# Performance work log

Measured on AMD Instinct MI355X. Metric: run time of the kernel, lower is better.

The kernel has to match this reference:

```python
import jax, jax.numpy as jnp
import numpy as np

BETA = 0.9      # LIF leak
THRESH = 1.0    # snntorch Leaky default threshold
SLOPE = 25.0    # fast_sigmoid surrogate slope

@jax.custom_vjp
def spike(x):
    # Heaviside forward, fast_sigmoid surrogate backward
    return (x > 0).astype(x.dtype)

def _spike_fwd(x):
    return spike(x), x

def _spike_bwd(x, g):
    return (g / (SLOPE * jnp.abs(x) + 1.0) ** 2,)

spike.defvjp(_spike_fwd, _spike_bwd)


def setup_inputs() -> dict:
    key = jax.random.key(0)
    k0, k1, k2, k3, k4 = jax.random.split(key, 5)
    B, T, I, H, C = 256, 100, 512, 1024, 8
    x = jax.random.normal(k0, (B, T, I), dtype=jnp.float32)
    s1 = 1.0 / np.sqrt(I)
    s2 = 1.0 / np.sqrt(H)
    W1 = jax.random.uniform(k1, (H, I), jnp.float32, -s1, s1)
    b1 = jax.random.uniform(k2, (H,), jnp.float32, -s1, s1)
    W2 = jax.random.uniform(k3, (C, H), jnp.float32, -s2, s2)
    b2 = jax.random.uniform(k4, (C,), jnp.float32, -s2, s2)
    return {"x": x, "W1": W1, "b1": b1, "W2": W2, "b2": b2}


def reference(x, W1, b1, W2, b2):
    # x: [B, T, I]
    B, T, I = x.shape
    H = W1.shape[0]
    # fc1 for all timesteps as one big GEMM (same math as per-step loop).
    cur = jnp.einsum('bti,hi->tbh', x, W1) + b1  # [T, B, H]

    def step(mem, c):
        # snntorch Leaky (reset_mechanism='subtract'):
        reset = spike(mem - THRESH)
        mem_new = BETA * mem + c - reset * THRESH
        spk = spike(mem_new - THRESH)
        return mem_new, spk

    mem0 = jnp.zeros((B, H), dtype=x.dtype)
    _, spk_rec = jax.lax.scan(step, mem0, cur)  # spk_rec: [T, B, H]

    # sum_t (spk_t @ W2.T + b2) == (sum_t spk_t) @ W2.T + T*b2
    spk_sum = spk_rec.sum(axis=0)  # [B, H]
    logits = spk_sum @ W2.T + T * b2  # [B, C]
    return logits
```

## Files before the change

kernel.cpp:

```cpp
#include <hip/hip_runtime.h>


#define B_   256
#define T_   100
#define I_   512
#define H_   1024
#define C_   8
#define M_   (B_ * T_)
#define KS_  1024
#define SC   64.0f
#define ISC  (1.0f / 4096.0f)
#define CP   132

typedef _Float16 half8 __attribute__((ext_vector_type(8)));
typedef float floatx4 __attribute__((ext_vector_type(4)));

__device__ __forceinline__ void ld_g2l(const _Float16* g, _Float16* l) {
    __builtin_amdgcn_global_load_lds(
        (const __attribute__((address_space(1))) void*)g,
        (__attribute__((address_space(3))) void*)l, 16, 0, 0);
}

__global__ void __launch_bounds__(256)
split_all(const float* __restrict__ x, const float* __restrict__ W1,
          const float* __restrict__ b2, _Float16* __restrict__ Asp,
          float* __restrict__ out) {
    int g = blockIdx.x * 256 + threadIdx.x;
    if (g < B_ * C_) out[g] = 100.0f * b2[g & (C_ - 1)];
    int row = g >> 6;
    int i0 = (g & 63) * 8;
    const float* src = (row < M_) ? (x + (size_t)row * I_ + i0)
                                  : (W1 + (size_t)(row - M_) * I_ + i0);
    float4 v0 = *(const float4*)(src);
    float4 v1 = *(const float4*)(src + 4);
    float vv[8] = {v0.x, v0.y, v0.z, v0.w, v1.x, v1.y, v1.z, v1.w};
    half8 hi, lo;
#pragma unroll
    for (int j = 0; j < 8; ++j) {
        float s = vv[j] * SC;
        _Float16 h = (_Float16)s;
        hi[j] = h;
        lo[j] = (_Float16)(s - (float)h);
    }
    _Float16* r = Asp + (size_t)row * KS_ + i0;
    *(half8*)(r) = hi;
    *(half8*)(r + 512) = lo;
}

__global__ void __launch_bounds__(256, 4)
snn_mfma(const _Float16* __restrict__ Asp, const _Float16* __restrict__ Wsp,
         const float* __restrict__ b1, const float* __restrict__ W2,
         float* __restrict__ logits) {
    __shared__ union {
        struct { __align__(16) _Float16 A[128 * 64]; __align__(16) _Float16 Bm[128 * 64]; } g;
        float Cs[64 * CP];
    } sm;
    const int tid = threadIdx.x;
    const int lane = tid & 63;
    const int w = tid >> 6;

    const int xcd = blockIdx.x & 7;
    const int jj = blockIdx.x >> 3;
    const int b  = xcd * 32 + (jj >> 3);
    const int n0 = (jj & 7) * 128;

    const int wm = (w >> 1) * 64;
    const int wn = (w & 1) * 64;
    const int srow = lane >> 3;
    const int sc16 = (lane & 7) ^ srow;

    const _Float16* ag[4];
    const _Float16* bg[4];
    _Float16* al[4];
    _Float16* bl[4];
#pragma unroll
    for (int j = 0; j < 4; ++j) {
        const int r = w * 32 + j * 8 + srow;
        ag[j] = Asp + ((size_t)b * T_ + r) * KS_ + sc16 * 8;
        bg[j] = Wsp + (size_t)(n0 + r) * KS_ + sc16 * 8;
        al[j] = &sm.g.A[(w * 32 + j * 8) * 64];
        bl[j] = &sm.g.Bm[(w * 32 + j * 8) * 64];
    }

    floatx4 acc[4][4];
#pragma unroll
    for (int i = 0; i < 4; ++i)
#pragma unroll
        for (int q = 0; q < 4; ++q) acc[i][q] = (floatx4){0.f, 0.f, 0.f, 0.f};

    const int quad = lane >> 4;
    const int l15 = lane & 15;
    const int l7 = lane & 7;

    for (int kt = 0; kt < 24; ++kt) {
        const int koA = ((kt & 16) ? 512 : 0) + (kt & 7) * 64;
        const int koB = ((kt & 8)  ? 512 : 0) + (kt & 7) * 64;
        __syncthreads();
#pragma unroll
        for (int j = 0; j < 4; ++j) {
            if (j < 2 || w < 3) ld_g2l(ag[j] + koA, al[j]);
            ld_g2l(bg[j] + koB, bl[j]);
        }
        __syncthreads();
#pragma unroll
        for (int ks = 0; ks < 2; ++ks) {
            const int c16 = (ks * 4 + quad) ^ l7;
            half8 av[3], bv[4];
#pragma unroll
            for (int f = 0; f < 3; ++f)
                av[f] = *(const half8*)&sm.g.A[(wm + f * 16 + l15) * 64 + c16 * 8];
#pragma unroll
            for (int f = 0; f < 4; ++f)
                bv[f] = *(const half8*)&sm.g.Bm[(wn + f * 16 + l15) * 64 + c16 * 8];
#pragma unroll
            for (int fr = 0; fr < 3; ++fr)
#pragma unroll
                for (int fn = 0; fn < 4; ++fn)
                    acc[fr][fn] = __builtin_amdgcn_mfma_f32_16x16x32_f16(
                        av[fr], bv[fn], acc[fr][fn], 0, 0, 0);
            if (wm == 0) {
                half8 a3 = *(const half8*)&sm.g.A[(48 + l15) * 64 + c16 * 8];
#pragma unroll
                for (int fn = 0; fn < 4; ++fn)
                    acc[3][fn] = __builtin_amdgcn_mfma_f32_16x16x32_f16(
                        a3, bv[fn], acc[3][fn], 0, 0, 0);
            }
        }
    }

    float b1c[4];
#pragma unroll
    for (int fn = 0; fn < 4; ++fn) b1c[fn] = b1[n0 + wn + fn * 16 + l15];

    float mem = 0.f, ss = 0.f;
    const int myh = tid & 127;

    __syncthreads();
    if (w < 2) {
#pragma unroll
        for (int fr = 0; fr < 4; ++fr)
#pragma unroll
            for (int r = 0; r < 4; ++r) {
                float* dst = &sm.Cs[(fr * 16 + quad * 4 + r) * CP + wn + l15];
#pragma unroll
                for (int fn = 0; fn < 4; ++fn)
                    dst[fn * 16] = acc[fr][fn][r] * ISC + b1c[fn];
            }
    }
    __syncthreads();
    if (tid < 128) {
#pragma unroll 8
        for (int t = 0; t < 64; ++t) {
            float c = sm.Cs[t * CP + myh];
            float reset = (mem > 1.0f) ? 1.0f : 0.0f;
            mem = 0.9f * mem + c - reset;
            ss += (mem > 1.0f) ? 1.0f : 0.0f;
        }
    }
    __syncthreads();
    if (w >= 2) {
#pragma unroll
        for (int fr = 0; fr < 3; ++fr)
#pragma unroll
            for (int r = 0; r < 4; ++r) {
                float* dst = &sm.Cs[(fr * 16 + quad * 4 + r) * CP + wn + l15];
#pragma unroll
                for (int fn = 0; fn < 4; ++fn)
                    dst[fn * 16] = acc[fr][fn][r] * ISC + b1c[fn];
            }
    }
    __syncthreads();
    if (tid < 128) {
#pragma unroll 6
        for (int t = 0; t < 36; ++t) {
            float c = sm.Cs[t * CP + myh];
            float reset = (mem > 1.0f) ? 1.0f : 0.0f;
            mem = 0.9f * mem + c - reset;
            ss += (mem > 1.0f) ? 1.0f : 0.0f;
        }
#pragma unroll
        for (int c = 0; c < C_; ++c) {
            float v = ss * W2[c * H_ + n0 + myh];
#pragma unroll
            for (int off = 32; off; off >>= 1) v += __shfl_down(v, off, 64);
            if (lane == 0) atomicAdd(&logits[b * C_ + c], v);
        }
    }
}

extern "C" void kernel_launch(void* const* d_in, const int* in_sizes, int n_in,
                              void* d_out, int out_size, void* d_ws, size_t ws_size,
                              hipStream_t stream) {
    const float* x  = (const float*)d_in[0];
    const float* W1 = (const float*)d_in[1];
    const float* b1 = (const float*)d_in[2];
    const float* W2 = (const float*)d_in[3];
    const float* b2 = (const float*)d_in[4];
    float* out = (float*)d_out;

    char* ws = (char*)d_ws;
    _Float16* Asp = (_Float16*)ws;
    _Float16* Wsp = (_Float16*)(ws + (size_t)M_ * KS_ * 2);

    hipLaunchKernelGGL(split_all, dim3((M_ + H_) * 64 / 256), dim3(256), 0, stream,
                       x, W1, b2, Asp, out);
    hipLaunchKernelGGL(snn_mfma, dim3(B_ * 8), dim3(256), 0, stream,
                       Asp, Wsp, b1, W2, out);
}
```

Before: 196.5 us.

## Use 32x32 MFMA with 128x256 tiles and double-buffered LDS pipeline

Replaces the 16x16x32 MFMA GEMM with 32x32x16 instructions over a wider 128x256 output tile per block, halving the grid. Global-to-LDS loads are double buffered with explicit waitcnt and barriers so the next K slice streams in while the current one computes. The split-fp16 product now loads hi and lo halves in the same stage and skips the lo*lo term in registers, instead of iterating 24 separate K tiles. All 256 threads run the LIF scan over 256 hidden units. Occupancy drops to 2 blocks per CU and register pressure rises.

```diff
diff --git a/kernel.cpp b/kernel.cpp
--- a/kernel.cpp
+++ b/kernel.cpp
@@ -10,10 +10,9 @@
 #define KS_  1024
 #define SC   64.0f
 #define ISC  (1.0f / 4096.0f)
-#define CP   132
 
 typedef _Float16 half8 __attribute__((ext_vector_type(8)));
-typedef float floatx4 __attribute__((ext_vector_type(4)));
+typedef float floatx16 __attribute__((ext_vector_type(16)));
 
 __device__ __forceinline__ void ld_g2l(const _Float16* g, _Float16* l) {
     __builtin_amdgcn_global_load_lds(
@@ -47,13 +46,50 @@
     *(half8*)(r + 512) = lo;
 }
 
-__global__ void __launch_bounds__(256, 4)
+#define MFMA32(A, Bv, Cacc) \
+    Cacc = __builtin_amdgcn_mfma_f32_32x32x16_f16(A, Bv, Cacc, 0, 0, 0)
+
+#define STAGE(dd, koff) do {                                         \
+    _Float16* lb = &sm.buf[0][0] + (dd) * 12288;                     \
+    ld_g2l(ga0 + (koff), lb + w * 512);                              \
+    ld_g2l(ga1 + (koff), lb + 2048 + w * 512);                       \
+    ld_g2l(gb00 + (koff), lb + 4096 + w * 1024);                     \
+    ld_g2l(gb01 + (koff), lb + 4096 + w * 1024 + 512);               \
+    ld_g2l(gb10 + (koff), lb + 8192 + w * 1024);                     \
+    ld_g2l(gb11 + (koff), lb + 8192 + w * 1024 + 512);               \
+} while (0)
+
+#define COMPUTE(dd) do {                                             \
+    const _Float16* bb = &sm.buf[0][0] + (dd) * 12288;               \
+    half8 ah[2], al[2], bh[4], bl[4];                                \
+    _Pragma("unroll")                                                \
+    for (int f = 0; f < 2; ++f) {                                    \
+        ah[f] = *(const half8*)(bb + ra + f * 512);                  \
+        al[f] = *(const half8*)(bb + 2048 + ra + f * 512);           \
+    }                                                                \
+    _Pragma("unroll")                                                \
+    for (int f = 0; f < 4; ++f) {                                    \
+        bh[f] = *(const half8*)(bb + 4096 + rb + f * 512);           \
+        bl[f] = *(const half8*)(bb + 8192 + rb + f * 512);           \
+    }                                                                \
+    _Pragma("unroll")                                                \
+    for (int fm = 0; fm < 2; ++fm) {                                 \
+        _Pragma("unroll")                                            \
+        for (int fn = 0; fn < 4; ++fn) {                             \
+            MFMA32(ah[fm], bh[fn], acc[fm][fn]);                     \
+            MFMA32(ah[fm], bl[fn], acc[fm][fn]);                     \
+            MFMA32(al[fm], bh[fn], acc[fm][fn]);                     \
+        }                                                            \
+    }                                                                \
+} while (0)
+
+__global__ void __launch_bounds__(256, 2)
 snn_mfma(const _Float16* __restrict__ Asp, const _Float16* __restrict__ Wsp,
          const float* __restrict__ b1, const float* __restrict__ W2,
          float* __restrict__ logits) {
     __shared__ union {
-        struct { __align__(16) _Float16 A[128 * 64]; __align__(16) _Float16 Bm[128 * 64]; } g;
-        float Cs[64 * CP];
+        __align__(16) _Float16 buf[2][12288];
+        float Cs[64 * 256];
     } sm;
     const int tid = threadIdx.x;
     const int lane = tid & 63;
@@ -61,130 +97,103 @@
 
     const int xcd = blockIdx.x & 7;
     const int jj = blockIdx.x >> 3;
-    const int b  = xcd * 32 + (jj >> 3);
-    const int n0 = (jj & 7) * 128;
+    const int b  = xcd * 32 + (jj >> 2);
+    const int n0 = (jj & 3) * 256;
 
     const int wm = (w >> 1) * 64;
-    const int wn = (w & 1) * 64;
-    const int srow = lane >> 3;
-    const int sc16 = (lane & 7) ^ srow;
-
-    const _Float16* ag[4];
-    const _Float16* bg[4];
-    _Float16* al[4];
-    _Float16* bl[4];
-#pragma unroll
-    for (int j = 0; j < 4; ++j) {
-        const int r = w * 32 + j * 8 + srow;
-        ag[j] = Asp + ((size_t)b * T_ + r) * KS_ + sc16 * 8;
-        bg[j] = Wsp + (size_t)(n0 + r) * KS_ + sc16 * 8;
-        al[j] = &sm.g.A[(w * 32 + j * 8) * 64];
-        bl[j] = &sm.g.Bm[(w * 32 + j * 8) * 64];
-    }
-
-    floatx4 acc[4][4];
-#pragma unroll
-    for (int i = 0; i < 4; ++i)
-#pragma unroll
-        for (int q = 0; q < 4; ++q) acc[i][q] = (floatx4){0.f, 0.f, 0.f, 0.f};
-
-    const int quad = lane >> 4;
-    const int l15 = lane & 15;
-    const int l7 = lane & 7;
-
-    for (int kt = 0; kt < 24; ++kt) {
-        const int koA = ((kt & 16) ? 512 : 0) + (kt & 7) * 64;
-        const int koB = ((kt & 8)  ? 512 : 0) + (kt & 7) * 64;
-        __syncthreads();
-#pragma unroll
-        for (int j = 0; j < 4; ++j) {
-            if (j < 2 || w < 3) ld_g2l(ag[j] + koA, al[j]);
-            ld_g2l(bg[j] + koB, bl[j]);
-        }
-        __syncthreads();
-#pragma unroll
-        for (int ks = 0; ks < 2; ++ks) {
-            const int c16 = (ks * 4 + quad) ^ l7;
-            half8 av[3], bv[4];
-#pragma unroll
-            for (int f = 0; f < 3; ++f)
-                av[f] = *(const half8*)&sm.g.A[(wm + f * 16 + l15) * 64 + c16 * 8];
-#pragma unroll
-            for (int f = 0; f < 4; ++f)
-                bv[f] = *(const half8*)&sm.g.Bm[(wn + f * 16 + l15) * 64 + c16 * 8];
-#pragma unroll
-            for (int fr = 0; fr < 3; ++fr)
+    const int wn = (w & 1) * 128;
+    const int l31 = lane & 31;
+    const int q2 = lane >> 5;
+
+    const int rl = lane >> 1;
+    const int cl8 = (lane & 1) * 8;
+    const _Float16* ga0 = Asp + (size_t)(b * T_ + w * 32 + rl) * KS_ + cl8;
+    const _Float16* ga1 = ga0 + 512;
+    const _Float16* gb00 = Wsp + (size_t)(n0 + w * 64 + rl) * KS_ + cl8;
+    const _Float16* gb01 = gb00 + 32 * KS_;
+    const _Float16* gb10 = gb00 + 512;
+    const _Float16* gb11 = gb01 + 512;
+
+    const int ra = (wm + l31) * 16 + q2 * 8;
+    const int rb = (wn + l31) * 16 + q2 * 8;
+
+    floatx16 acc[2][4];
+#pragma unroll
+    for (int i = 0; i < 2; ++i)
+#pragma unroll
+        for (int j = 0; j < 4; ++j)
+#pragma unroll
+            for (int e = 0; e < 16; ++e) acc[i][j][e] = 0.f;
+
+    STAGE(0, 0);
+#pragma unroll 2
+    for (int c = 0; c < 31; ++c) {
+        const int d = c & 1;
+        STAGE(d ^ 1, (c + 1) * 16);
+        asm volatile("s_waitcnt vmcnt(6)" ::: "memory");
+        __builtin_amdgcn_s_barrier();
+        COMPUTE(d);
+        __builtin_amdgcn_s_barrier();
+        asm volatile("" ::: "memory");
+    }
+    asm volatile("s_waitcnt vmcnt(0)" ::: "memory");
+    __builtin_amdgcn_s_barrier();
+    COMPUTE(1);
+    __syncthreads();
+
+    float b1c[4];
+#pragma unroll
+    for (int fn = 0; fn < 4; ++fn) b1c[fn] = b1[n0 + wn + fn * 32 + l31];
+
+    float mem = 0.f, ss = 0.f;
+
+    if (w < 2) {
+#pragma unroll
+        for (int fm = 0; fm < 2; ++fm)
+#pragma unroll
+            for (int r = 0; r < 16; ++r) {
+                const int row = fm * 32 + (r & 3) + 8 * (r >> 2) + 4 * q2;
+                float* dst = &sm.Cs[row * 256 + wn + l31];
 #pragma unroll
                 for (int fn = 0; fn < 4; ++fn)
-                    acc[fr][fn] = __builtin_amdgcn_mfma_f32_16x16x32_f16(
-                        av[fr], bv[fn], acc[fr][fn], 0, 0, 0);
-            if (wm == 0) {
-                half8 a3 = *(const half8*)&sm.g.A[(48 + l15) * 64 + c16 * 8];
+                    dst[fn * 32] = acc[fm][fn][r] * ISC + b1c[fn];
+            }
+    }
+    __syncthreads();
+#pragma unroll 8
+    for (int t = 0; t < 64; ++t) {
+        float cv = sm.Cs[t * 256 + tid];
+        float reset = (mem > 1.0f) ? 1.0f : 0.0f;
+        mem = 0.9f * mem + cv - reset;
+        ss += (mem > 1.0f) ? 1.0f : 0.0f;
+    }
+    __syncthreads();
+    if (w >= 2) {
+#pragma unroll
+        for (int fm = 0; fm < 2; ++fm)
+#pragma unroll
+            for (int r = 0; r < 16; ++r) {
+                const int row = fm * 32 + (r & 3) + 8 * (r >> 2) + 4 * q2;
+                float* dst = &sm.Cs[row * 256 + wn + l31];
 #pragma unroll
                 for (int fn = 0; fn < 4; ++fn)
-                    acc[3][fn] = __builtin_amdgcn_mfma_f32_16x16x32_f16(
-                        a3, bv[fn], acc[3][fn], 0, 0, 0);
+                    dst[fn * 32] = acc[fm][fn][r] * ISC + b1c[fn];
             }
-        }
-    }
-
-    float b1c[4];
-#pragma unroll
-    for (int fn = 0; fn < 4; ++fn) b1c[fn] = b1[n0 + wn + fn * 16 + l15];
-
-    float mem = 0.f, ss = 0.f;
-    const int myh = tid & 127;
-
-    __syncthreads();
-    if (w < 2) {
-#pragma unroll
-        for (int fr = 0; fr < 4; ++fr)
-#pragma unroll
-            for (int r = 0; r < 4; ++r) {
-                float* dst = &sm.Cs[(fr * 16 + quad * 4 + r) * CP + wn + l15];
-#pragma unroll
-                for (int fn = 0; fn < 4; ++fn)
-                    dst[fn * 16] = acc[fr][fn][r] * ISC + b1c[fn];
-            }
-    }
-    __syncthreads();
-    if (tid < 128) {
-#pragma unroll 8
-        for (int t = 0; t < 64; ++t) {
-            float c = sm.Cs[t * CP + myh];
-            float reset = (mem > 1.0f) ? 1.0f : 0.0f;
-            mem = 0.9f * mem + c - reset;
-            ss += (mem > 1.0f) ? 1.0f : 0.0f;
-        }
-    }
-    __syncthreads();
-    if (w >= 2) {
-#pragma unroll
-        for (int fr = 0; fr < 3; ++fr)
-#pragma unroll
-            for (int r = 0; r < 4; ++r) {
-                float* dst = &sm.Cs[(fr * 16 + quad * 4 + r) * CP + wn + l15];
-#pragma unroll
-                for (int fn = 0; fn < 4; ++fn)
-                    dst[fn * 16] = acc[fr][fn][r] * ISC + b1c[fn];
-            }
-    }
-    __syncthreads();
-    if (tid < 128) {
+    }
+    __syncthreads();
 #pragma unroll 6
-        for (int t = 0; t < 36; ++t) {
-            float c = sm.Cs[t * CP + myh];
-            float reset = (mem > 1.0f) ? 1.0f : 0.0f;
-            mem = 0.9f * mem + c - reset;
-            ss += (mem > 1.0f) ? 1.0f : 0.0f;
-        }
-#pragma unroll
-        for (int c = 0; c < C_; ++c) {
-            float v = ss * W2[c * H_ + n0 + myh];
-#pragma unroll
-            for (int off = 32; off; off >>= 1) v += __shfl_down(v, off, 64);
-            if (lane == 0) atomicAdd(&logits[b * C_ + c], v);
-        }
+    for (int t = 0; t < 36; ++t) {
+        float cv = sm.Cs[t * 256 + tid];
+        float reset = (mem > 1.0f) ? 1.0f : 0.0f;
+        mem = 0.9f * mem + cv - reset;
+        ss += (mem > 1.0f) ? 1.0f : 0.0f;
+    }
+#pragma unroll
+    for (int cc = 0; cc < C_; ++cc) {
+        float v = ss * W2[cc * H_ + n0 + tid];
+#pragma unroll
+        for (int off = 32; off; off >>= 1) v += __shfl_down(v, off, 64);
+        if (lane == 0) atomicAdd(&logits[b * C_ + cc], v);
     }
 }
 
@@ -204,6 +213,6 @@
 
     hipLaunchKernelGGL(split_all, dim3((M_ + H_) * 64 / 256), dim3(256), 0, stream,
                        x, W1, b2, Asp, out);
-    hipLaunchKernelGGL(snn_mfma, dim3(B_ * 8), dim3(256), 0, stream,
+    hipLaunchKernelGGL(snn_mfma, dim3(B_ * 4), dim3(256), 0, stream,
                        Asp, Wsp, b1, W2, out);
 }
```

After: 216.4 us. 1.1x slower.
